# Optimization experiments

Hardware: AMD Instinct MI355X
Metric: run time of the kernel (lower is better)

The kernel has to match this reference:

```python
import jax, jax.numpy as jnp
import numpy as np

LN_EPS = 1e-5

def _layernorm(x, g, b):
    mu = jnp.mean(x, axis=-1, keepdims=True)
    var = jnp.mean(jnp.square(x - mu), axis=-1, keepdims=True)
    return (x - mu) * jax.lax.rsqrt(var + LN_EPS) * g + b

def setup_inputs() -> dict:
    key = jax.random.key(0)
    ks = jax.random.split(key, 8)
    B, T, C = 4, 2048, 1024
    s = 0.02
    return {
        "x": jax.random.normal(ks[0], (B, T, C), jnp.float32),
        "w_qkv": jax.random.normal(ks[1], (C, 3 * C), jnp.float32) * s,
        "b_qkv": jnp.zeros((3 * C,), jnp.float32),
        "w_out": jax.random.normal(ks[2], (C, C), jnp.float32) * s,
        "b_out": jnp.zeros((C,), jnp.float32),
        "w1": jax.random.normal(ks[3], (C, 4 * C), jnp.float32) * s,
        "b1": jnp.zeros((4 * C,), jnp.float32),
        "w2": jax.random.normal(ks[4], (4 * C, C), jnp.float32) * s,
        "b2": jnp.zeros((C,), jnp.float32),
        "g1": jnp.ones((C,), jnp.float32),
        "be1": jnp.zeros((C,), jnp.float32),
        "g2": jnp.ones((C,), jnp.float32),
        "be2": jnp.zeros((C,), jnp.float32),
        "n_head": 16,
    }

def reference(x, w_qkv, b_qkv, w_out, b_out, w1, b1, w2, b2, g1, be1, g2, be2, n_head):
    B, T, C = x.shape
    H = n_head
    D = C // H
    # --- causal self-attention ---
    qkv = x @ w_qkv + b_qkv                      # [B,T,3C]
    q, k, v = jnp.split(qkv, 3, axis=-1)
    q = q.reshape(B, T, H, D).transpose(0, 2, 1, 3)  # [B,H,T,D]
    k = k.reshape(B, T, H, D).transpose(0, 2, 1, 3)
    v = v.reshape(B, T, H, D).transpose(0, 2, 1, 3)
    attn = jnp.einsum("bhqd,bhkd->bhqk", q, k) * (1.0 / np.sqrt(D))
    causal = jnp.tril(jnp.ones((T, T), bool))
    attn = jnp.where(causal, attn, jnp.float32(-jnp.inf))
    attn = jax.nn.softmax(attn, axis=-1)
    y = jnp.einsum("bhqk,bhkd->bhqd", attn, v)
    y = y.transpose(0, 2, 1, 3).reshape(B, T, C)
    y = y @ w_out + b_out
    # post-norm residual (norm applied to sublayer output)
    x = x + _layernorm(y, g1, be1)
    # --- MLP ---
    h = jax.nn.gelu(x @ w1 + b1, approximate=False)
    h = h @ w2 + b2
    x = x + _layernorm(h, g2, be2)
    return x
```

## Files before the change

kernel.cpp:

```cpp
#include <hip/hip_runtime.h>
#include <hip/hip_bf16.h>

typedef unsigned short ushort_t;
using bf16x8 = __attribute__((ext_vector_type(8))) short;
using f32x4  = __attribute__((ext_vector_type(4))) float;

#define DEV __device__ __forceinline__

DEV unsigned short f2bf(float f) {
    unsigned int u = __builtin_bit_cast(unsigned int, f);
    u = (u + 0x7fffu + ((u >> 16) & 1u)) >> 16;
    return (unsigned short)u;
}

DEV int cvtpk_bf16(float lo, float hi) {
    int r;
    asm("v_cvt_pk_bf16_f32 %0, %1, %2" : "=v"(r) : "v"(lo), "v"(hi));
    return r;
}

DEV void gload16(const unsigned short* g, unsigned short* l) {
    __builtin_amdgcn_global_load_lds(
        (const __attribute__((address_space(1))) void*)g,
        (__attribute__((address_space(3))) void*)l, 16, 0, 0);
}

DEV float gelu_f(float v) {
    float u = v * (0.79788456f + 0.03567741f * v * v);
    float t = __builtin_amdgcn_exp2f(u * 2.88539008f);
    return v * t * __builtin_amdgcn_rcpf(t + 1.0f);
}

__global__ __launch_bounds__(256) void cvtbf_kernel(const float* __restrict__ in,
                                                    unsigned short* __restrict__ out) {
    int i = (blockIdx.x * 256 + threadIdx.x) * 4;
    float4 v = *(const float4*)&in[i];
    out[i + 0] = f2bf(v.x);
    out[i + 1] = f2bf(v.y);
    out[i + 2] = f2bf(v.z);
    out[i + 3] = f2bf(v.w);
}

__global__ __launch_bounds__(256) void transpose_cvt_kernel(const float* __restrict__ in,
                                                            unsigned short* __restrict__ out,
                                                            int R, int C) {
    __shared__ float t[32][33];
    int tx = threadIdx.x, ty = threadIdx.y;
    int c0 = blockIdx.x * 32, r0 = blockIdx.y * 32;
#pragma unroll
    for (int i = 0; i < 4; ++i)
        t[ty + i * 8][tx] = in[(size_t)(r0 + ty + i * 8) * C + c0 + tx];
    __syncthreads();
#pragma unroll
    for (int i = 0; i < 4; ++i)
        out[(size_t)(c0 + ty + i * 8) * R + r0 + tx] = f2bf(t[tx][ty + i * 8]);
}

__global__ __launch_bounds__(256) void vtrans_kernel(const unsigned short* __restrict__ qkvb,
                                                     unsigned short* __restrict__ vtg) {
    __shared__ unsigned short t[64 * 66];
    const int tid = threadIdx.x;
    const int t0 = blockIdx.x * 64;
    const int bh = blockIdx.y;
    const int b = bh >> 4, h = bh & 15;
    const unsigned short* src = qkvb + (size_t)(b * 2048 + t0) * 3072 + 2048 + h * 64;
#pragma unroll
    for (int c = 0; c < 2; ++c) {
        int cid = c * 256 + tid;
        int row = cid >> 3, cc = cid & 7;
        *(int4*)&t[row * 66 + cc * 8] = *(const int4*)&src[(size_t)row * 3072 + cc * 8];
    }
    __syncthreads();
    unsigned short* dst = vtg + (size_t)bh * 64 * 2048 + t0;
#pragma unroll
    for (int c = 0; c < 2; ++c) {
        int cid = c * 256 + tid;
        int d = cid >> 3, cc2 = cid & 7;
        bf16x8 v;
#pragma unroll
        for (int j = 0; j < 8; ++j) v[j] = (short)t[(cc2 * 8 + j) * 66 + d];
        *(bf16x8*)&dst[(size_t)d * 2048 + cc2 * 8] = v;
    }
}

template <int ACT, int OBF>
__global__ __launch_bounds__(512) void gemm256_kernel(
    const unsigned short* __restrict__ A, const unsigned short* __restrict__ Bt,
    const float* __restrict__ bias, void* __restrict__ out, void* __restrict__ out2,
    int N, int Ktot, int gridNt, int GM, int nSlices) {
    __shared__ __align__(16) unsigned short lA[2][16384];
    __shared__ __align__(16) unsigned short lB[2][16384];
    const int tid = threadIdx.x;
    const int lane = tid & 63, wid = tid >> 6;
    const int g = lane >> 4, lr = lane & 15;
    const int wm = wid >> 2, wn = wid & 3;

    const int nwg = gridDim.x, cpx = nwg >> 3, bid = blockIdx.x;
    const int wkid = (bid & 7) * cpx + (bid >> 3);
    const int bps = nwg / nSlices;
    const int sl = wkid / bps, rem = wkid % bps;
    const int mt = (rem / (GM * gridNt)) * GM + (rem % GM);
    const int nt = (rem / GM) % gridNt;
    const int m0 = mt * 256, n0 = nt * 256;
    const int Ksl = Ktot / nSlices;
    const int kbase = sl * Ksl;
    const int nkt = Ksl >> 6;
    void* outp = (sl == 0) ? out : out2;

    auto stageA = [&](int kh, int kt, int bb) {
#pragma unroll
        for (int s = 0; s < 2; ++s) {
            int c = s * 512 + tid;
            int row = c & 255, kb = kh * 4 + (c >> 8);
            gload16(&A[(size_t)(m0 + row) * Ktot + kbase + kt * 64 + kb * 8],
                    &lA[bb][(size_t)(kh * 1024 + s * 512 + (tid & ~63)) * 8]);
        }
    };
    auto stageB = [&](int kh, int kt, int bb) {
#pragma unroll
        for (int s = 0; s < 2; ++s) {
            int c = s * 512 + tid;
            int row = c & 255, kb = kh * 4 + (c >> 8);
            gload16(&Bt[(size_t)(n0 + row) * Ktot + kbase + kt * 64 + kb * 8],
                    &lB[bb][(size_t)(kh * 1024 + s * 512 + (tid & ~63)) * 8]);
        }
    };

    f32x4 acc[8][4] = {};
    bf16x8 bfr[4];

    stageA(0, 0, 0); stageB(0, 0, 0);
    stageA(1, 0, 0); stageB(1, 0, 0);
    if (nkt > 1) { stageA(0, 1, 1); stageB(0, 1, 1); }

    for (int u = 0; u < nkt; ++u) {
        const int buf = u & 1;
        const bool tail = (u >= nkt - 2);
#pragma unroll
        for (int p = 0; p < 4; ++p) {
            const int ks = p >> 1, mh = p & 1;
            if (mh == 0) {
                if (tail) asm volatile("s_waitcnt vmcnt(0)" ::: "memory");
                else      asm volatile("s_waitcnt vmcnt(8)" ::: "memory");
                __builtin_amdgcn_s_barrier();
                asm volatile("" ::: "memory");
            }
            bf16x8 af[4];
#pragma unroll
            for (int mf2 = 0; mf2 < 4; ++mf2) {
                int ci = (ks * 4 + g) * 256 + wm * 128 + (mh * 4 + mf2) * 16 + lr;
                af[mf2] = *(const bf16x8*)&lA[buf][(size_t)ci * 8];
            }
            if (mh == 0) {
#pragma unroll
                for (int nf = 0; nf < 4; ++nf) {
                    int ci = (ks * 4 + g) * 256 + wn * 64 + nf * 16 + lr;
                    bfr[nf] = *(const bf16x8*)&lB[buf][(size_t)ci * 8];
                }
            }
            if (p == 0)      { if (u + 1 < nkt) stageA(1, u + 1, buf ^ 1); }
            else if (p == 1) { if (u + 1 < nkt) stageB(1, u + 1, buf ^ 1); }
            else if (p == 2) { if (u + 2 < nkt) stageA(0, u + 2, buf); }
            else             { if (u + 2 < nkt) stageB(0, u + 2, buf); }
            __builtin_amdgcn_s_barrier();
            asm volatile("s_waitcnt lgkmcnt(0)" ::: "memory");
            __builtin_amdgcn_sched_barrier(0);
            __builtin_amdgcn_s_setprio(1);
#pragma unroll
            for (int mf2 = 0; mf2 < 4; ++mf2)
#pragma unroll
                for (int nf = 0; nf < 4; ++nf)
                    acc[mh * 4 + mf2][nf] = __builtin_amdgcn_mfma_f32_16x16x32_bf16(
                        af[mf2], bfr[nf], acc[mh * 4 + mf2][nf], 0, 0, 0);
            __builtin_amdgcn_s_setprio(0);
            __builtin_amdgcn_sched_barrier(0);
            __builtin_amdgcn_s_barrier();
            asm volatile("" ::: "memory");
        }
    }

#pragma unroll
    for (int mf = 0; mf < 8; ++mf) {
#pragma unroll
        for (int nf = 0; nf < 4; ++nf) {
            int col = n0 + wn * 64 + nf * 16 + lr;
            float bv = (sl == 0) ? bias[col] : 0.0f;
#pragma unroll
            for (int r = 0; r < 4; ++r) {
                int row = m0 + wm * 128 + mf * 16 + g * 4 + r;
                float v = acc[mf][nf][r] + bv;
                if (ACT == 1) v = gelu_f(v);
                if (OBF)
                    ((unsigned short*)outp)[(size_t)row * N + col] = f2bf(v);
                else
                    ((float*)outp)[(size_t)row * N + col] = v;
            }
        }
    }
}

__global__ __launch_bounds__(256, 2) void attn_kernel(const unsigned short* __restrict__ qkv,
                                                      const unsigned short* __restrict__ vtg,
                                                      unsigned short* __restrict__ y) {
    __shared__ unsigned short Kl[2][128 * 64];
    __shared__ unsigned short Vl[2][64 * 128];
    const int tid = threadIdx.x, lane = tid & 63, w = tid >> 6;
    const int g = lane >> 4, lr = lane & 15;
    const int id = blockIdx.x + 8 * (blockIdx.y + 16 * blockIdx.z);
    const int xcd = id & 7, wrk = id >> 3;
    const int bh = xcd * 8 + (wrk & 7);
    const int p = wrk >> 3;
    const int b = bh >> 4, h = bh & 15;
    const size_t rs3 = 3072;
    const unsigned short* qbase = qkv + (size_t)b * 2048 * rs3 + h * 64;
    const unsigned short* kbase = qbase + 1024;
    const unsigned short* vbase = vtg + (size_t)bh * 64 * 2048;

    int ksoff[4], vsoff[4], ldoff[4];
#pragma unroll
    for (int c = 0; c < 4; ++c) {
        int cid = c * 256 + tid;
        int krow = cid >> 3, kcc = cid & 7;
        ksoff[c] = krow * 3072 + (kcc ^ (krow & 7) ^ ((krow >> 3) & 7)) * 8;
        int d = cid >> 4, tcs = cid & 15;
        vsoff[c] = d * 2048 + (tcs ^ ((d & 7) ^ ((d >> 3) & 7))) * 8;
        ldoff[c] = (c * 256 + (tid & ~63)) * 8;
    }

    const int idxP0 = 4 * (32 * (g & 1) + lr);
    const int idxP1 = idxP0 + 64;
    int idxA[4];
#pragma unroll
    for (int r = 0; r < 4; ++r) idxA[r] = 4 * (g * 20 + r);
    const bool ghigh = (g >> 1) != 0;
    const float qscale = 0.125f * 1.44269504089f;

    auto process = [&](int J) {
        const int q0w = J * 128 + w * 32;
        const int ktend = J + 1;
#pragma unroll
        for (int c = 0; c < 4; ++c) {
            gload16(&kbase[ksoff[c]], &Kl[0][ldoff[c]]);
            gload16(&vbase[vsoff[c]], &Vl[0][ldoff[c]]);
        }
        int qf[2][2][4];
#pragma unroll
        for (int sub = 0; sub < 2; ++sub)
#pragma unroll
            for (int f = 0; f < 2; ++f) {
                int4 v = *(const int4*)&qbase[(size_t)(q0w + sub * 16 + lr) * rs3 + f * 32 + g * 8];
                int vv[4] = {v.x, v.y, v.z, v.w};
#pragma unroll
                for (int i = 0; i < 4; ++i) {
                    unsigned int u = (unsigned int)vv[i];
                    float lo = __builtin_bit_cast(float, u << 16) * qscale;
                    float hi = __builtin_bit_cast(float, u & 0xffff0000u) * qscale;
                    qf[sub][f][i] = cvtpk_bf16(lo, hi);
                }
            }

        f32x4 O[2][4] = {};
        float m_[2] = {-3.0e38f, -3.0e38f}, l_[2] = {0.f, 0.f};

        int buf = 0;
        for (int kt = 0; kt < ktend; ++kt) {
            asm volatile("s_waitcnt vmcnt(0)" ::: "memory");
            __builtin_amdgcn_s_barrier();
            asm volatile("" ::: "memory");
            if (kt + 1 < ktend) {
#pragma unroll
                for (int c = 0; c < 4; ++c) {
                    gload16(&kbase[(size_t)(kt + 1) * 128 * 3072 + ksoff[c]], &Kl[buf ^ 1][ldoff[c]]);
                    gload16(&vbase[vsoff[c] + (kt + 1) * 128], &Vl[buf ^ 1][ldoff[c]]);
                }
            }
            const unsigned short* Kc = Kl[buf];
            const unsigned short* Vc = Vl[buf];

            f32x4 s0[8], s1[8];
#pragma unroll
            for (int st = 0; st < 8; ++st) {
                int rbase = (st * 16 + lr) * 64;
                int sw = (lr & 7) ^ ((st * 2 + (lr >> 3)) & 7);
                bf16x8 kf0 = *(const bf16x8*)&Kc[rbase + ((g ^ sw) * 8)];
                bf16x8 kf1 = *(const bf16x8*)&Kc[rbase + (((4 + g) ^ sw) * 8)];
                f32x4 a = {};
                a = __builtin_amdgcn_mfma_f32_16x16x32_bf16(kf0, *(const bf16x8*)&qf[0][0], a, 0, 0, 0);
                a = __builtin_amdgcn_mfma_f32_16x16x32_bf16(kf1, *(const bf16x8*)&qf[0][1], a, 0, 0, 0);
                s0[st] = a;
                f32x4 c = {};
                c = __builtin_amdgcn_mfma_f32_16x16x32_bf16(kf0, *(const bf16x8*)&qf[1][0], c, 0, 0, 0);
                c = __builtin_amdgcn_mfma_f32_16x16x32_bf16(kf1, *(const bf16x8*)&qf[1][1], c, 0, 0, 0);
                s1[st] = c;
            }

            int wt0[4][4], wt1[4][4];
#pragma unroll
            for (int sub = 0; sub < 2; ++sub) {
                f32x4* s = (sub == 0) ? s0 : s1;
                const int qmin = q0w + sub * 16;
                if (kt == J) {
                    int qv = qmin + lr;
#pragma unroll
                    for (int st = 0; st < 8; ++st) {
                        int keyb = kt * 128 + st * 16 + g * 4;
#pragma unroll
                        for (int r = 0; r < 4; ++r)
                            if (keyb + r > qv) s[st][r] = -3.0e38f;
                    }
                }
                float mx = fmaxf(fmaxf(s[0][0], s[0][1]), fmaxf(s[0][2], s[0][3]));
#pragma unroll
                for (int st = 1; st < 8; ++st)
                    mx = fmaxf(mx, fmaxf(fmaxf(s[st][0], s[st][1]), fmaxf(s[st][2], s[st][3])));
                mx = fmaxf(mx, __shfl_xor(mx, 16));
                mx = fmaxf(mx, __shfl_xor(mx, 32));
                if (__any(mx - m_[sub] > 11.5f)) {
                    float mnew = fmaxf(m_[sub], mx);
                    float alpha = __builtin_amdgcn_exp2f(m_[sub] - mnew);
                    m_[sub] = mnew;
                    l_[sub] *= alpha;
                    int av = __builtin_bit_cast(int, alpha);
                    f32x4* Os = O[sub];
#pragma unroll
                    for (int r = 0; r < 4; ++r) {
                        float ar = __builtin_bit_cast(float, __builtin_amdgcn_ds_bpermute(idxA[r], av));
#pragma unroll
                        for (int dt = 0; dt < 4; ++dt) Os[dt][r] *= ar;
                    }
                }
                float rs = 0.f;
#pragma unroll
                for (int st = 0; st < 8; ++st)
#pragma unroll
                    for (int r = 0; r < 4; ++r) {
                        float pp = __builtin_amdgcn_exp2f(s[st][r] - m_[sub]);
                        s[st][r] = pp;
                        rs += pp;
                    }
                rs += __shfl_xor(rs, 16);
                rs += __shfl_xor(rs, 32);
                l_[sub] += rs;
                int ws_[8][2];
#pragma unroll
                for (int st = 0; st < 8; ++st) {
                    ws_[st][0] = cvtpk_bf16(s[st][0], s[st][1]);
                    ws_[st][1] = cvtpk_bf16(s[st][2], s[st][3]);
                }
                int(*wt)[4] = (sub == 0) ? wt0 : wt1;
#pragma unroll
                for (int ks = 0; ks < 4; ++ks)
#pragma unroll
                    for (int hp = 0; hp < 4; ++hp) {
                        int idx = (hp < 2) ? idxP0 : idxP1;
                        int v0 = __builtin_amdgcn_ds_bpermute(idx, ws_[2 * ks][hp & 1]);
                        int v1 = __builtin_amdgcn_ds_bpermute(idx, ws_[2 * ks + 1][hp & 1]);
                        wt[ks][hp] = ghigh ? v1 : v0;
                    }
            }

#pragma unroll
            for (int ks = 0; ks < 4; ++ks) {
                bf16x8 pa0 = *(const bf16x8*)&wt0[ks][0];
                bf16x8 pa1 = *(const bf16x8*)&wt1[ks][0];
#pragma unroll
                for (int dt = 0; dt < 4; ++dt) {
                    int d = dt * 16 + lr;
                    int tc = (ks * 4 + g) ^ ((lr & 7) ^ ((dt * 2 + (lr >> 3)) & 7));
                    bf16x8 vf = *(const bf16x8*)&Vc[d * 128 + tc * 8];
                    O[0][dt] = __builtin_amdgcn_mfma_f32_16x16x32_bf16(pa0, vf, O[0][dt], 0, 0, 0);
                    O[1][dt] = __builtin_amdgcn_mfma_f32_16x16x32_bf16(pa1, vf, O[1][dt], 0, 0, 0);
                }
            }
            buf ^= 1;
        }

#pragma unroll
        for (int sub = 0; sub < 2; ++sub) {
            int lv = __builtin_bit_cast(int, l_[sub]);
#pragma unroll
            for (int r = 0; r < 4; ++r) {
                float lval = __builtin_bit_cast(float, __builtin_amdgcn_ds_bpermute(idxA[r], lv));
                float inv = __builtin_amdgcn_rcpf(lval);
                int q = q0w + sub * 16 + g * 4 + r;
#pragma unroll
                for (int dt = 0; dt < 4; ++dt)
                    y[(size_t)(b * 2048 + q) * 1024 + h * 64 + dt * 16 + lr] =
                        f2bf(O[sub][dt][r] * inv);
            }
        }
    };

    process(15 - p);
    __syncthreads();
    process(p);
}

template <int WRITE_BF>
__global__ __launch_bounds__(256) void ln_kernel(const float* __restrict__ base,
                                                 const float* __restrict__ delta,
                                                 const float* __restrict__ delta2,
                                                 const float* __restrict__ gw,
                                                 const float* __restrict__ bw,
                                                 float* __restrict__ outf,
                                                 unsigned short* __restrict__ outb) {
    const int row = blockIdx.x;
    const int tid = threadIdx.x;
    const float* d = delta + (size_t)row * 1024;
    const float* bs = base + (size_t)row * 1024;
    float4 x = *(const float4*)&d[tid * 4];
    if (delta2) {
        float4 x2 = *(const float4*)&delta2[(size_t)row * 1024 + tid * 4];
        x.x += x2.x; x.y += x2.y; x.z += x2.z; x.w += x2.w;
    }
    float s = x.x + x.y + x.z + x.w;
    float s2 = x.x * x.x + x.y * x.y + x.z * x.z + x.w * x.w;
#pragma unroll
    for (int off = 1; off < 64; off <<= 1) {
        s += __shfl_xor(s, off);
        s2 += __shfl_xor(s2, off);
    }
    __shared__ float red[8];
    if ((tid & 63) == 0) {
        red[tid >> 6] = s;
        red[4 + (tid >> 6)] = s2;
    }
    __syncthreads();
    s = red[0] + red[1] + red[2] + red[3];
    s2 = red[4] + red[5] + red[6] + red[7];
    float mu = s * (1.f / 1024.f);
    float var = s2 * (1.f / 1024.f) - mu * mu;
    float rsig = rsqrtf(var + 1e-5f);
    float4 bb = *(const float4*)&bs[tid * 4];
    float4 gv = *(const float4*)&gw[tid * 4];
    float4 bv = *(const float4*)&bw[tid * 4];
    float4 o;
    o.x = bb.x + (x.x - mu) * rsig * gv.x + bv.x;
    o.y = bb.y + (x.y - mu) * rsig * gv.y + bv.y;
    o.z = bb.z + (x.z - mu) * rsig * gv.z + bv.z;
    o.w = bb.w + (x.w - mu) * rsig * gv.w + bv.w;
    *(float4*)&outf[(size_t)row * 1024 + tid * 4] = o;
    if (WRITE_BF) {
        unsigned short* ob = outb + (size_t)row * 1024 + tid * 4;
        ob[0] = f2bf(o.x);
        ob[1] = f2bf(o.y);
        ob[2] = f2bf(o.z);
        ob[3] = f2bf(o.w);
    }
}

extern "C" void kernel_launch(void* const* d_in, const int* in_sizes, int n_in,
                              void* d_out, int out_size, void* d_ws, size_t ws_size,
                              hipStream_t stream) {
    const float* x = (const float*)d_in[0];
    const float* w_qkv = (const float*)d_in[1];
    const float* b_qkv = (const float*)d_in[2];
    const float* w_out = (const float*)d_in[3];
    const float* b_out = (const float*)d_in[4];
    const float* w1 = (const float*)d_in[5];
    const float* b1 = (const float*)d_in[6];
    const float* w2 = (const float*)d_in[7];
    const float* b2 = (const float*)d_in[8];
    const float* g1 = (const float*)d_in[9];
    const float* be1 = (const float*)d_in[10];
    const float* g2 = (const float*)d_in[11];
    const float* be2 = (const float*)d_in[12];

    const size_t MB = 1ull << 20;
    if (ws_size < 184 * MB) return;
    char* ws = (char*)d_ws;
    unsigned short* xb    = (unsigned short*)(ws + 0);
    unsigned short* vtg   = (unsigned short*)(ws + 0);
    float*          attnp1= (float*)(ws + 0);
    unsigned short* wqkvt = (unsigned short*)(ws + 16 * MB);
    unsigned short* qkvb  = (unsigned short*)(ws + 22 * MB);
    float*          ff1   = (float*)(ws + 22 * MB);
    unsigned short* hb    = (unsigned short*)(ws + 0);
    unsigned short* woutt = (unsigned short*)(ws + 70 * MB);
    unsigned short* yb    = (unsigned short*)(ws + 72 * MB);
    float*          attnp = (float*)(ws + 88 * MB);
    float*          ff    = (float*)(ws + 88 * MB);
    float*          x2f   = (float*)(ws + 120 * MB);
    unsigned short* x2b   = (unsigned short*)(ws + 152 * MB);
    unsigned short* w1t   = (unsigned short*)(ws + 168 * MB);
    unsigned short* w2t   = (unsigned short*)(ws + 176 * MB);

    cvtbf_kernel<<<8192, 256, 0, stream>>>(x, xb);
    transpose_cvt_kernel<<<dim3(96, 32), dim3(32, 8), 0, stream>>>(w_qkv, wqkvt, 1024, 3072);
    transpose_cvt_kernel<<<dim3(32, 32), dim3(32, 8), 0, stream>>>(w_out, woutt, 1024, 1024);
    transpose_cvt_kernel<<<dim3(128, 32), dim3(32, 8), 0, stream>>>(w1, w1t, 1024, 4096);
    transpose_cvt_kernel<<<dim3(32, 128), dim3(32, 8), 0, stream>>>(w2, w2t, 4096, 1024);
    gemm256_kernel<0, 1><<<384, 512, 0, stream>>>(xb, wqkvt, b_qkv, qkvb, nullptr,
                                                  3072, 1024, 12, 4, 1);
    vtrans_kernel<<<dim3(32, 64), 256, 0, stream>>>(qkvb, vtg);
    attn_kernel<<<dim3(8, 16, 4), 256, 0, stream>>>(qkvb, vtg, yb);
    gemm256_kernel<0, 0><<<256, 512, 0, stream>>>(yb, woutt, b_out, attnp, attnp1,
                                                  1024, 1024, 4, 8, 2);
    ln_kernel<1><<<8192, 256, 0, stream>>>(x, attnp, attnp1, g1, be1, x2f, x2b);
    gemm256_kernel<1, 1><<<512, 512, 0, stream>>>(x2b, w1t, b1, hb, nullptr,
                                                  4096, 1024, 16, 4, 1);
    gemm256_kernel<0, 0><<<256, 512, 0, stream>>>(hb, w2t, b2, ff, ff1,
                                                  1024, 4096, 4, 8, 2);
    ln_kernel<0><<<8192, 256, 0, stream>>>(x2f, ff, ff1, g2, be2, (float*)d_out, nullptr);
}
```

Before: 481.1 us.

## Restructure GEMM main loop to whole-tile double buffering with register-prefetched fragments

Replaces the four-phase half-tile staging pipeline, which had multiple barriers per k-step, with a simpler double-buffered scheme. The whole next 64-wide k-tile of A and B is issued at the start of each iteration, and LDS fragment reads are interleaved with MFMA groups through ping-pong register sets. Only one vmcnt(0) wait and one barrier remain per iteration, which cuts synchronisation overhead. In exchange the prefetch distance drops from roughly two half-steps to one full tile, so global-load latency may be exposed at the end of each iteration, and the extra fragment registers raise register pressure.

```diff
diff --git a/kernel.cpp b/kernel.cpp
--- a/kernel.cpp
+++ b/kernel.cpp
@@ -107,76 +107,88 @@
     const int nkt = Ksl >> 6;
     void* outp = (sl == 0) ? out : out2;
 
-    auto stageA = [&](int kh, int kt, int bb) {
-#pragma unroll
-        for (int s = 0; s < 2; ++s) {
+    auto stageAll = [&](int kt, int bb) {
+#pragma unroll
+        for (int s = 0; s < 4; ++s) {
             int c = s * 512 + tid;
-            int row = c & 255, kb = kh * 4 + (c >> 8);
+            int row = c & 255, kb = c >> 8;
             gload16(&A[(size_t)(m0 + row) * Ktot + kbase + kt * 64 + kb * 8],
-                    &lA[bb][(size_t)(kh * 1024 + s * 512 + (tid & ~63)) * 8]);
+                    &lA[bb][(size_t)(s * 512 + (tid & ~63)) * 8]);
+        }
+#pragma unroll
+        for (int s = 0; s < 4; ++s) {
+            int c = s * 512 + tid;
+            int row = c & 255, kb = c >> 8;
+            gload16(&Bt[(size_t)(n0 + row) * Ktot + kbase + kt * 64 + kb * 8],
+                    &lB[bb][(size_t)(s * 512 + (tid & ~63)) * 8]);
         }
     };
-    auto stageB = [&](int kh, int kt, int bb) {
-#pragma unroll
-        for (int s = 0; s < 2; ++s) {
-            int c = s * 512 + tid;
-            int row = c & 255, kb = kh * 4 + (c >> 8);
-            gload16(&Bt[(size_t)(n0 + row) * Ktot + kbase + kt * 64 + kb * 8],
-                    &lB[bb][(size_t)(kh * 1024 + s * 512 + (tid & ~63)) * 8]);
+
+    auto readAf = [&](int ks, int mh, int buf, bf16x8* af) {
+#pragma unroll
+        for (int mf2 = 0; mf2 < 4; ++mf2) {
+            int ci = (ks * 4 + g) * 256 + wm * 128 + (mh * 4 + mf2) * 16 + lr;
+            af[mf2] = *(const bf16x8*)&lA[buf][(size_t)ci * 8];
         }
     };
+    auto readBf = [&](int ks, int buf, bf16x8* bf_) {
+#pragma unroll
+        for (int nf = 0; nf < 4; ++nf) {
+            int ci = (ks * 4 + g) * 256 + wn * 64 + nf * 16 + lr;
+            bf_[nf] = *(const bf16x8*)&lB[buf][(size_t)ci * 8];
+        }
+    };
 
     f32x4 acc[8][4] = {};
-    bf16x8 bfr[4];
-
-    stageA(0, 0, 0); stageB(0, 0, 0);
-    stageA(1, 0, 0); stageB(1, 0, 0);
-    if (nkt > 1) { stageA(0, 1, 1); stageB(0, 1, 1); }
-
-    for (int u = 0; u < nkt; ++u) {
-        const int buf = u & 1;
-        const bool tail = (u >= nkt - 2);
-#pragma unroll
-        for (int p = 0; p < 4; ++p) {
-            const int ks = p >> 1, mh = p & 1;
-            if (mh == 0) {
-                if (tail) asm volatile("s_waitcnt vmcnt(0)" ::: "memory");
-                else      asm volatile("s_waitcnt vmcnt(8)" ::: "memory");
-                __builtin_amdgcn_s_barrier();
-                asm volatile("" ::: "memory");
-            }
-            bf16x8 af[4];
-#pragma unroll
-            for (int mf2 = 0; mf2 < 4; ++mf2) {
-                int ci = (ks * 4 + g) * 256 + wm * 128 + (mh * 4 + mf2) * 16 + lr;
-                af[mf2] = *(const bf16x8*)&lA[buf][(size_t)ci * 8];
-            }
-            if (mh == 0) {
-#pragma unroll
-                for (int nf = 0; nf < 4; ++nf) {
-                    int ci = (ks * 4 + g) * 256 + wn * 64 + nf * 16 + lr;
-                    bfr[nf] = *(const bf16x8*)&lB[buf][(size_t)ci * 8];
-                }
-            }
-            if (p == 0)      { if (u + 1 < nkt) stageA(1, u + 1, buf ^ 1); }
-            else if (p == 1) { if (u + 1 < nkt) stageB(1, u + 1, buf ^ 1); }
-            else if (p == 2) { if (u + 2 < nkt) stageA(0, u + 2, buf); }
-            else             { if (u + 2 < nkt) stageB(0, u + 2, buf); }
-            __builtin_amdgcn_s_barrier();
-            asm volatile("s_waitcnt lgkmcnt(0)" ::: "memory");
-            __builtin_amdgcn_sched_barrier(0);
-            __builtin_amdgcn_s_setprio(1);
-#pragma unroll
-            for (int mf2 = 0; mf2 < 4; ++mf2)
-#pragma unroll
-                for (int nf = 0; nf < 4; ++nf)
-                    acc[mh * 4 + mf2][nf] = __builtin_amdgcn_mfma_f32_16x16x32_bf16(
-                        af[mf2], bfr[nf], acc[mh * 4 + mf2][nf], 0, 0, 0);
-            __builtin_amdgcn_s_setprio(0);
-            __builtin_amdgcn_sched_barrier(0);
-            __builtin_amdgcn_s_barrier();
-            asm volatile("" ::: "memory");
-        }
+    bf16x8 afA[4], afB[4], bfrA[4], bfrB[4];
+
+    stageAll(0, 0);
+    asm volatile("s_waitcnt vmcnt(0)" ::: "memory");
+    __builtin_amdgcn_s_barrier();
+    asm volatile("" ::: "memory");
+
+    for (int kt = 0; kt < nkt; ++kt) {
+        const int buf = kt & 1;
+        if (kt + 1 < nkt) stageAll(kt + 1, buf ^ 1);
+        readAf(0, 0, buf, afA);
+        readBf(0, buf, bfrA);
+        readAf(0, 1, buf, afB);
+        __builtin_amdgcn_s_setprio(1);
+#pragma unroll
+        for (int mf2 = 0; mf2 < 4; ++mf2)
+#pragma unroll
+            for (int nf = 0; nf < 4; ++nf)
+                acc[mf2][nf] = __builtin_amdgcn_mfma_f32_16x16x32_bf16(
+                    afA[mf2], bfrA[nf], acc[mf2][nf], 0, 0, 0);
+        __builtin_amdgcn_s_setprio(0);
+        readAf(1, 0, buf, afA);
+        readBf(1, buf, bfrB);
+        __builtin_amdgcn_s_setprio(1);
+#pragma unroll
+        for (int mf2 = 0; mf2 < 4; ++mf2)
+#pragma unroll
+            for (int nf = 0; nf < 4; ++nf)
+                acc[4 + mf2][nf] = __builtin_amdgcn_mfma_f32_16x16x32_bf16(
+                    afB[mf2], bfrA[nf], acc[4 + mf2][nf], 0, 0, 0);
+        __builtin_amdgcn_s_setprio(0);
+        readAf(1, 1, buf, afB);
+        __builtin_amdgcn_s_setprio(1);
+#pragma unroll
+        for (int mf2 = 0; mf2 < 4; ++mf2)
+#pragma unroll
+            for (int nf = 0; nf < 4; ++nf)
+                acc[mf2][nf] = __builtin_amdgcn_mfma_f32_16x16x32_bf16(
+                    afA[mf2], bfrB[nf], acc[mf2][nf], 0, 0, 0);
+#pragma unroll
+        for (int mf2 = 0; mf2 < 4; ++mf2)
+#pragma unroll
+            for (int nf = 0; nf < 4; ++nf)
+                acc[4 + mf2][nf] = __builtin_amdgcn_mfma_f32_16x16x32_bf16(
+                    afB[mf2], bfrB[nf], acc[4 + mf2][nf], 0, 0, 0);
+        __builtin_amdgcn_s_setprio(0);
+        asm volatile("s_waitcnt vmcnt(0)" ::: "memory");
+        __builtin_amdgcn_s_barrier();
+        asm volatile("" ::: "memory");
     }
 
 #pragma unroll
```

New measurement: 565.6 us. 1.18x slower.

## Restructure GEMM double-buffer pipeline, cheapen GELU, and write bf16 split-K partials

Applied to the files above, without the earlier changes.

Reworks the 256x256 GEMM prefetch schedule so each full next k-tile loads into the alternate LDS buffer during the current tile, with waits moved after the MFMA phases. It also adds a min-blocks-per-CU of 2 to the launch bounds. The second split-K partial of the MLP down-projection is now written as bf16 and read back in the LayerNorm, cutting that buffer's traffic. GELU changes from the tanh form to the cruder x*sigmoid(1.702x) approximation, which saves arithmetic but adds numerical error. The occupancy hint may force register spills, since the accumulators alone fill the register budget it implies, and LDS use likely cannot fit two blocks anyway.

```diff
diff --git a/kernel.cpp b/kernel.cpp
--- a/kernel.cpp
+++ b/kernel.cpp
@@ -13,6 +13,10 @@
     return (unsigned short)u;
 }
 
+DEV float bf2f(unsigned short s) {
+    return __builtin_bit_cast(float, (unsigned int)s << 16);
+}
+
 DEV int cvtpk_bf16(float lo, float hi) {
     int r;
     asm("v_cvt_pk_bf16_f32 %0, %1, %2" : "=v"(r) : "v"(lo), "v"(hi));
@@ -26,8 +30,7 @@
 }
 
 DEV float gelu_f(float v) {
-    float u = v * (0.79788456f + 0.03567741f * v * v);
-    float t = __builtin_amdgcn_exp2f(u * 2.88539008f);
+    float t = __builtin_amdgcn_exp2f(v * 2.4554946f);
     return v * t * __builtin_amdgcn_rcpf(t + 1.0f);
 }
 
@@ -83,13 +86,13 @@
     }
 }
 
-template <int ACT, int OBF>
-__global__ __launch_bounds__(512) void gemm256_kernel(
+template <int ACT, int OBF, int OBF2>
+__global__ __launch_bounds__(512, 2) void gemm256_kernel(
     const unsigned short* __restrict__ A, const unsigned short* __restrict__ Bt,
     const float* __restrict__ bias, void* __restrict__ out, void* __restrict__ out2,
     int N, int Ktot, int gridNt, int GM, int nSlices) {
-    __shared__ __align__(16) unsigned short lA[2][16384];
-    __shared__ __align__(16) unsigned short lB[2][16384];
+    __shared__ __align__(16) unsigned short lA[2][256 * 64];
+    __shared__ __align__(16) unsigned short lB[2][256 * 64];
     const int tid = threadIdx.x;
     const int lane = tid & 63, wid = tid >> 6;
     const int g = lane >> 4, lr = lane & 15;
@@ -103,65 +106,57 @@
     const int nt = (rem / GM) % gridNt;
     const int m0 = mt * 256, n0 = nt * 256;
     const int Ksl = Ktot / nSlices;
-    const int kbase = sl * Ksl;
+    const int kb0 = sl * Ksl;
     const int nkt = Ksl >> 6;
     void* outp = (sl == 0) ? out : out2;
 
-    auto stageA = [&](int kh, int kt, int bb) {
-#pragma unroll
-        for (int s = 0; s < 2; ++s) {
-            int c = s * 512 + tid;
-            int row = c & 255, kb = kh * 4 + (c >> 8);
-            gload16(&A[(size_t)(m0 + row) * Ktot + kbase + kt * 64 + kb * 8],
-                    &lA[bb][(size_t)(kh * 1024 + s * 512 + (tid & ~63)) * 8]);
-        }
+    auto stageA = [&](int s, int kt, int bb) {
+        int c = s * 512 + tid;
+        int row = c & 255, kb = c >> 8;
+        gload16(&A[(size_t)(m0 + row) * Ktot + kb0 + kt * 64 + kb * 8],
+                &lA[bb][(size_t)(s * 512 + (tid & ~63)) * 8]);
     };
-    auto stageB = [&](int kh, int kt, int bb) {
-#pragma unroll
-        for (int s = 0; s < 2; ++s) {
-            int c = s * 512 + tid;
-            int row = c & 255, kb = kh * 4 + (c >> 8);
-            gload16(&Bt[(size_t)(n0 + row) * Ktot + kbase + kt * 64 + kb * 8],
-                    &lB[bb][(size_t)(kh * 1024 + s * 512 + (tid & ~63)) * 8]);
-        }
+    auto stageB = [&](int s, int kt, int bb) {
+        int c = s * 512 + tid;
+        int row = c & 255, kb = c >> 8;
+        gload16(&Bt[(size_t)(n0 + row) * Ktot + kb0 + kt * 64 + kb * 8],
+                &lB[bb][(size_t)(s * 512 + (tid & ~63)) * 8]);
     };
 
     f32x4 acc[8][4] = {};
     bf16x8 bfr[4];
 
-    stageA(0, 0, 0); stageB(0, 0, 0);
-    stageA(1, 0, 0); stageB(1, 0, 0);
-    if (nkt > 1) { stageA(0, 1, 1); stageB(0, 1, 1); }
-
-    for (int u = 0; u < nkt; ++u) {
-        const int buf = u & 1;
-        const bool tail = (u >= nkt - 2);
+    stageA(0, 0, 0); stageA(1, 0, 0); stageB(0, 0, 0); stageB(1, 0, 0);
+    stageA(2, 0, 0); stageA(3, 0, 0); stageB(2, 0, 0); stageB(3, 0, 0);
+    asm volatile("s_waitcnt vmcnt(4)" ::: "memory");
+    __builtin_amdgcn_s_barrier();
+    asm volatile("" ::: "memory");
+
+    for (int kt = 0; kt < nkt; ++kt) {
+        const int buf = kt & 1;
+        const bool more = (kt + 1 < nkt);
 #pragma unroll
         for (int p = 0; p < 4; ++p) {
             const int ks = p >> 1, mh = p & 1;
+            bf16x8 af[4];
+#pragma unroll
+            for (int mf2 = 0; mf2 < 4; ++mf2) {
+                int c = (ks * 4 + g) * 256 + wm * 128 + (mh * 4 + mf2) * 16 + lr;
+                af[mf2] = *(const bf16x8*)&lA[buf][(size_t)c * 8];
+            }
             if (mh == 0) {
-                if (tail) asm volatile("s_waitcnt vmcnt(0)" ::: "memory");
-                else      asm volatile("s_waitcnt vmcnt(8)" ::: "memory");
-                __builtin_amdgcn_s_barrier();
-                asm volatile("" ::: "memory");
-            }
-            bf16x8 af[4];
-#pragma unroll
-            for (int mf2 = 0; mf2 < 4; ++mf2) {
-                int ci = (ks * 4 + g) * 256 + wm * 128 + (mh * 4 + mf2) * 16 + lr;
-                af[mf2] = *(const bf16x8*)&lA[buf][(size_t)ci * 8];
-            }
-            if (mh == 0) {
 #pragma unroll
                 for (int nf = 0; nf < 4; ++nf) {
-                    int ci = (ks * 4 + g) * 256 + wn * 64 + nf * 16 + lr;
-                    bfr[nf] = *(const bf16x8*)&lB[buf][(size_t)ci * 8];
-                }
-            }
-            if (p == 0)      { if (u + 1 < nkt) stageA(1, u + 1, buf ^ 1); }
-            else if (p == 1) { if (u + 1 < nkt) stageB(1, u + 1, buf ^ 1); }
-            else if (p == 2) { if (u + 2 < nkt) stageA(0, u + 2, buf); }
-            else             { if (u + 2 < nkt) stageB(0, u + 2, buf); }
+                    int c = (ks * 4 + g) * 256 + wn * 64 + nf * 16 + lr;
+                    bfr[nf] = *(const bf16x8*)&lB[buf][(size_t)c * 8];
+                }
+            }
+            if (more) {
+                if (p == 0)      { stageA(0, kt + 1, buf ^ 1); stageA(1, kt + 1, buf ^ 1); }
+                else if (p == 1) { stageB(0, kt + 1, buf ^ 1); stageB(1, kt + 1, buf ^ 1); }
+                else if (p == 2) { stageA(2, kt + 1, buf ^ 1); stageA(3, kt + 1, buf ^ 1); }
+                else             { stageB(2, kt + 1, buf ^ 1); stageB(3, kt + 1, buf ^ 1); }
+            }
             __builtin_amdgcn_s_barrier();
             asm volatile("s_waitcnt lgkmcnt(0)" ::: "memory");
             __builtin_amdgcn_sched_barrier(0);
@@ -174,6 +169,12 @@
                         af[mf2], bfr[nf], acc[mh * 4 + mf2][nf], 0, 0, 0);
             __builtin_amdgcn_s_setprio(0);
             __builtin_amdgcn_sched_barrier(0);
+            if (p == 1) {
+                if (more) asm volatile("s_waitcnt vmcnt(4)" ::: "memory");
+                else      asm volatile("s_waitcnt vmcnt(0)" ::: "memory");
+            } else if (p == 3) {
+                if (more) asm volatile("s_waitcnt vmcnt(4)" ::: "memory");
+            }
             __builtin_amdgcn_s_barrier();
             asm volatile("" ::: "memory");
         }
@@ -190,10 +191,17 @@
                 int row = m0 + wm * 128 + mf * 16 + g * 4 + r;
                 float v = acc[mf][nf][r] + bv;
                 if (ACT == 1) v = gelu_f(v);
-                if (OBF)
-                    ((unsigned short*)outp)[(size_t)row * N + col] = f2bf(v);
-                else
-                    ((float*)outp)[(size_t)row * N + col] = v;
+                if (sl == 0) {
+                    if (OBF)
+                        ((unsigned short*)outp)[(size_t)row * N + col] = f2bf(v);
+                    else
+                        ((float*)outp)[(size_t)row * N + col] = v;
+                } else {
+                    if (OBF2)
+                        ((unsigned short*)outp)[(size_t)row * N + col] = f2bf(v);
+                    else
+                        ((float*)outp)[(size_t)row * N + col] = v;
+                }
             }
         }
     }
@@ -396,10 +404,10 @@
     process(p);
 }
 
-template <int WRITE_BF>
+template <int WRITE_BF, int D2BF>
 __global__ __launch_bounds__(256) void ln_kernel(const float* __restrict__ base,
                                                  const float* __restrict__ delta,
-                                                 const float* __restrict__ delta2,
+                                                 const void* __restrict__ delta2,
                                                  const float* __restrict__ gw,
                                                  const float* __restrict__ bw,
                                                  float* __restrict__ outf,
@@ -409,8 +417,13 @@
     const float* d = delta + (size_t)row * 1024;
     const float* bs = base + (size_t)row * 1024;
     float4 x = *(const float4*)&d[tid * 4];
-    if (delta2) {
-        float4 x2 = *(const float4*)&delta2[(size_t)row * 1024 + tid * 4];
+    if (D2BF) {
+        const unsigned short* d2 = (const unsigned short*)delta2 + (size_t)row * 1024 + tid * 4;
+        ushort4 u = *(const ushort4*)d2;
+        x.x += bf2f(u.x); x.y += bf2f(u.y); x.z += bf2f(u.z); x.w += bf2f(u.w);
+    } else {
+        const float* d2 = (const float*)delta2 + (size_t)row * 1024 + tid * 4;
+        float4 x2 = *(const float4*)d2;
         x.x += x2.x; x.y += x2.y; x.z += x2.z; x.w += x2.w;
     }
     float s = x.x + x.y + x.z + x.w;
@@ -472,12 +485,12 @@
     unsigned short* xb    = (unsigned short*)(ws + 0);
     unsigned short* vtg   = (unsigned short*)(ws + 0);
     float*          attnp1= (float*)(ws + 0);
+    unsigned short* hb    = (unsigned short*)(ws + 0);
     unsigned short* wqkvt = (unsigned short*)(ws + 16 * MB);
     unsigned short* qkvb  = (unsigned short*)(ws + 22 * MB);
-    float*          ff1   = (float*)(ws + 22 * MB);
-    unsigned short* hb    = (unsigned short*)(ws + 0);
     unsigned short* woutt = (unsigned short*)(ws + 70 * MB);
     unsigned short* yb    = (unsigned short*)(ws + 72 * MB);
+    unsigned short* ff1b  = (unsigned short*)(ws + 72 * MB);
     float*          attnp = (float*)(ws + 88 * MB);
     float*          ff    = (float*)(ws + 88 * MB);
     float*          x2f   = (float*)(ws + 120 * MB);
@@ -490,16 +503,16 @@
     transpose_cvt_kernel<<<dim3(32, 32), dim3(32, 8), 0, stream>>>(w_out, woutt, 1024, 1024);
     transpose_cvt_kernel<<<dim3(128, 32), dim3(32, 8), 0, stream>>>(w1, w1t, 1024, 4096);
     transpose_cvt_kernel<<<dim3(32, 128), dim3(32, 8), 0, stream>>>(w2, w2t, 4096, 1024);
-    gemm256_kernel<0, 1><<<384, 512, 0, stream>>>(xb, wqkvt, b_qkv, qkvb, nullptr,
-                                                  3072, 1024, 12, 4, 1);
+    gemm256_kernel<0, 1, 1><<<384, 512, 0, stream>>>(xb, wqkvt, b_qkv, qkvb, nullptr,
+                                                     3072, 1024, 12, 4, 1);
     vtrans_kernel<<<dim3(32, 64), 256, 0, stream>>>(qkvb, vtg);
     attn_kernel<<<dim3(8, 16, 4), 256, 0, stream>>>(qkvb, vtg, yb);
-    gemm256_kernel<0, 0><<<256, 512, 0, stream>>>(yb, woutt, b_out, attnp, attnp1,
-                                                  1024, 1024, 4, 8, 2);
-    ln_kernel<1><<<8192, 256, 0, stream>>>(x, attnp, attnp1, g1, be1, x2f, x2b);
-    gemm256_kernel<1, 1><<<512, 512, 0, stream>>>(x2b, w1t, b1, hb, nullptr,
-                                                  4096, 1024, 16, 4, 1);
-    gemm256_kernel<0, 0><<<256, 512, 0, stream>>>(hb, w2t, b2, ff, ff1,
-                                                  1024, 4096, 4, 8, 2);
-    ln_kernel<0><<<8192, 256, 0, stream>>>(x2f, ff, ff1, g2, be2, (float*)d_out, nullptr);
-}
+    gemm256_kernel<0, 0, 0><<<256, 512, 0, stream>>>(yb, woutt, b_out, attnp, attnp1,
+                                                     1024, 1024, 4, 8, 2);
+    ln_kernel<1, 0><<<8192, 256, 0, stream>>>(x, attnp, attnp1, g1, be1, x2f, x2b);
+    gemm256_kernel<1, 1, 1><<<512, 512, 0, stream>>>(x2b, w1t, b1, hb, nullptr,
+                                                     4096, 1024, 16, 4, 1);
+    gemm256_kernel<0, 0, 1><<<256, 512, 0, stream>>>(hb, w2t, b2, ff, ff1b,
+                                                     1024, 4096, 4, 8, 2);
+    ln_kernel<0, 1><<<8192, 256, 0, stream>>>(x2f, ff, ff1b, g2, be2, (float*)d_out, nullptr);
+}
```

Measured after the change: 465.8 us. 3.2% less time.
